# Kernel tuning notes

Measured on AMD Instinct MI355X. Metric: run time of the kernel, lower is better.

Reference implementation:

```python
import jax, jax.numpy as jnp
import numpy as np


def _lstm(x, Wx, Wh, b):
    """Fused-gate LSTM over time axis 1. x: [B,T,I]; Wx: [I,4H]; Wh: [H,4H]; b: [4H].
    Gate order (i, f, g, o) as in flax.linen.LSTMCell. Zero initial carry."""
    B, T, _ = x.shape
    H = Wh.shape[0]
    # Precompute all input-to-gate contributions in one big GEMM.
    xg = jnp.einsum('bti,ih->bth', x, Wx) + b  # [B,T,4H]

    def step(carry, xt):
        c, h = carry
        z = xt + h @ Wh  # [B,4H]
        i, f, g, o = jnp.split(z, 4, axis=-1)
        c = jax.nn.sigmoid(f) * c + jax.nn.sigmoid(i) * jnp.tanh(g)
        h = jax.nn.sigmoid(o) * jnp.tanh(c)
        return (c, h), h

    init = (jnp.zeros((B, H), x.dtype), jnp.zeros((B, H), x.dtype))
    _, hs = jax.lax.scan(step, init, jnp.swapaxes(xg, 0, 1))  # hs: [T,B,H]
    return jnp.swapaxes(hs, 0, 1)  # [B,T,H]


def _forward(X, conv_w, conv_b,
             Wx1, Wh1, b1, Wx2, Wh2, b2, Wx3, Wh3, b3, Wx4, Wh4, b4,
             Wa, ba, Va, bva, Wd1, bd1, Wd2, bd2):
    # 1-D conv, SAME padding (flax default), NWC layout.
    x = jax.lax.conv_general_dilated(X, conv_w, (1,), 'SAME',
                                     dimension_numbers=('NWC', 'WIO', 'NWC')) + conv_b
    # NOTE: source uses jnp.flip(..., axis=-1) -> flips FEATURE axis (faithful to source).
    x1 = _lstm(x, Wx1, Wh1, b1)
    x2 = _lstm(jnp.flip(x, axis=-1), Wx2, Wh2, b2)
    x = jnp.concatenate([x1, x2], axis=-1)  # [B,T,2F]
    x1 = _lstm(x, Wx3, Wh3, b3)
    x2 = _lstm(jnp.flip(x, axis=-1), Wx4, Wh4, b4)
    enc = jnp.concatenate([x1, x2], axis=-1)  # [B,T,4F]
    # Additive attention: softmax over time axis.
    score = jnp.tanh(enc @ Wa + ba) @ Va + bva  # [B,T,1]
    w = jax.nn.softmax(score, axis=1)
    ctx = jnp.sum(w * enc, axis=1)  # [B,4F]
    # MLP head (dropout deterministic -> identity).
    h = jnp.tanh(ctx @ Wd1 + bd1)
    return h @ Wd2 + bd2  # [B,1]


def setup_inputs() -> dict:
    key = jax.random.key(0)
    B, T, Cin, F = 32, 4096, 8, 64
    ks = iter(jax.random.split(key, 32))

    def w(shape):
        fan_in = shape[0] if len(shape) <= 2 else shape[0] * shape[1]
        return jax.random.normal(next(ks), shape, jnp.float32) / np.sqrt(fan_in)

    d = {}
    d['X'] = jax.random.normal(next(ks), (B, T, Cin), jnp.float32)
    d['conv_w'] = w((4, Cin, 16))
    d['conv_b'] = jnp.zeros((16,), jnp.float32)
    lstm_dims = {'1': (16, F), '2': (16, F), '3': (2 * F, 2 * F), '4': (2 * F, 2 * F)}
    for n, (i_dim, h_dim) in lstm_dims.items():
        d['Wx' + n] = w((i_dim, 4 * h_dim))
        d['Wh' + n] = w((h_dim, 4 * h_dim))
        d['b' + n] = jnp.zeros((4 * h_dim,), jnp.float32)
    d['Wa'] = w((4 * F, F)); d['ba'] = jnp.zeros((F,), jnp.float32)
    d['Va'] = w((F, 1));     d['bva'] = jnp.zeros((1,), jnp.float32)
    d['Wd1'] = w((4 * F, F)); d['bd1'] = jnp.zeros((F,), jnp.float32)
    d['Wd2'] = w((F, 1));     d['bd2'] = jnp.zeros((1,), jnp.float32)
    d['deterministic'] = 1
    return d


def reference(X, conv_w, conv_b,
              Wx1, Wh1, b1, Wx2, Wh2, b2, Wx3, Wh3, b3, Wx4, Wh4, b4,
              Wa, ba, Va, bva, Wd1, bd1, Wd2, bd2, deterministic):
    # deterministic=1 -> dropout is the identity; already reflected in _forward.
    return _forward(X, conv_w, conv_b,
                    Wx1, Wh1, b1, Wx2, Wh2, b2, Wx3, Wh3, b3, Wx4, Wh4, b4,
                    Wa, ba, Va, bva, Wd1, bd1, Wd2, bd2)
```

## Files before the change

### kernel.cpp

```cpp
#include <hip/hip_runtime.h>


#define TFULL 4096
#define NB 32

__device__ __forceinline__ float fexp2(float x){ return __builtin_amdgcn_exp2f(x); }
__device__ __forceinline__ float frcp(float x){ return __builtin_amdgcn_rcpf(x); }
__device__ __forceinline__ float sigf(float x){ return frcp(1.f + fexp2(-1.44269504f*x)); }
__device__ __forceinline__ float tanh_(float x){
    float e = fexp2(fminf(2.88539008f*x, 126.f));
    return (e - 1.f) * frcp(e + 1.f);
}
#define PIN4(v) asm volatile("" : "+v"(v.x), "+v"(v.y), "+v"(v.z), "+v"(v.w))

__global__ __launch_bounds__(256) void k_init(float* __restrict__ st1,
        float* __restrict__ st2, float* __restrict__ am, float* __restrict__ al,
        float* __restrict__ acc){
    int i = blockIdx.x * 256 + threadIdx.x;
    if (i < 8192)  st1[i] = 0.f;
    if (i < 16384) st2[i] = 0.f;
    if (i < 8192)  acc[i] = 0.f;
    if (i < 32){ am[i] = -3.4e38f; al[i] = 0.f; }
}

__global__ __launch_bounds__(256) void k_pack(
        const float* __restrict__ Wx1, const float* __restrict__ Wh1, const float* __restrict__ b1,
        const float* __restrict__ Wx2, const float* __restrict__ Wh2, const float* __restrict__ b2,
        const float* __restrict__ Wx3, const float* __restrict__ Wh3, const float* __restrict__ b3,
        const float* __restrict__ Wx4, const float* __restrict__ Wh4, const float* __restrict__ b4,
        float* __restrict__ W34, float* __restrict__ b34, float* __restrict__ W2p,
        float* __restrict__ W1p, float* __restrict__ b12){
    int i0 = blockIdx.x * 256 + threadIdx.x;
    int stride = gridDim.x * 256;
    for (int e = i0; e < 131072; e += stride){
        int k = e >> 10, n = e & 1023;
        W34[e] = (n < 512) ? Wx3[k*512 + n] : Wx4[(127 - k)*512 + (n - 512)];
    }
    for (int e = i0; e < 1024; e += stride) b34[e] = (e < 512) ? b3[e] : b4[e - 512];
    for (int e = i0; e < 131072; e += stride){
        int l = e >> 16, f = e & 65535;
        int p = f >> 14, g = f & 16383, tid = g >> 5, kk = g & 31;
        int q = tid & 127, s = tid >> 7;
        W2p[e] = (l ? Wh4 : Wh3)[(32*s + kk)*512 + 4*q + p];
    }
    for (int e = i0; e < 65536; e += stride){
        int l = e >> 15, r = e & 32767, tid = r >> 6, wq = r & 63;
        int q = tid & 63, s = tid >> 6;
        float v = 0.f;
        if (wq < 32){
            int c = wq >> 3, k = wq & 7;
            v = (l ? Wh2 : Wh1)[(s*8 + k)*256 + (4*q + c)];
        } else if (s < 2){
            int c = (wq - 32) >> 3, rr = (wq - 32) & 7;
            int rg = s*8 + rr, col = 4*q + c;
            v = l ? Wx2[(15 - rg)*256 + col] : Wx1[rg*256 + col];
        }
        W1p[e] = v;
    }
    for (int e = i0; e < 512; e += stride) b12[e] = (e < 256) ? b1[e] : b2[e - 256];
}

__global__ __launch_bounds__(256) void k_conv(const float* __restrict__ X,
        const float* __restrict__ W, const float* __restrict__ Bv,
        float* __restrict__ out, int t0, int lc){
    __shared__ float Ws[512];
    __shared__ float bs[16];
    int tid = threadIdx.x;
    Ws[tid] = W[tid]; Ws[tid + 256] = W[tid + 256];
    if (tid < 16) bs[tid] = Bv[tid];
    __syncthreads();
    int m = blockIdx.x * 256 + tid;
    int b = m >> lc, trel = m & ((1 << lc) - 1);
    int t = t0 + trel;
    float o[16];
    #pragma unroll
    for (int co = 0; co < 16; ++co) o[co] = bs[co];
    #pragma unroll
    for (int w = 0; w < 4; ++w){
        int tt = t + w - 1;
        if (tt >= 0 && tt < TFULL){
            const float* xr = X + ((size_t)(b << 12) + tt) * 8;
            #pragma unroll
            for (int ci = 0; ci < 8; ++ci){
                float v = xr[ci];
                #pragma unroll
                for (int co = 0; co < 16; ++co) o[co] += v * Ws[(w*8 + ci)*16 + co];
            }
        }
    }
    float* op = out + (size_t)m * 16;
    #pragma unroll
    for (int q = 0; q < 4; ++q)
        *(float4*)(op + q*4) = make_float4(o[q*4], o[q*4+1], o[q*4+2], o[q*4+3]);
}

__global__ void __launch_bounds__(512, 1)
k_scan1(const float* __restrict__ x, const float* __restrict__ W1p,
        const float* __restrict__ b12,
        float* __restrict__ cc, float* __restrict__ st1, int C){
    int l = blockIdx.x >> 5;
    int b = blockIdx.x & 31;
    int tid = threadIdx.x;
    int q = tid & 63;
    int s = tid >> 6;
    float4 w[16];
    {
        const float4* wp = (const float4*)(W1p + ((size_t)l*512 + tid)*64);
        #pragma unroll
        for (int i = 0; i < 16; ++i) w[i] = wp[i];
        #pragma unroll
        for (int i = 0; i < 16; ++i) PIN4(w[i]);
    }
    float bi0 = 0.f, bi1 = 0.f, bi2 = 0.f, bi3 = 0.f;
    if (tid < 64){
        bi0 = b12[l*256 + tid];       bi1 = b12[l*256 + 64 + tid];
        bi2 = b12[l*256 + 128 + tid]; bi3 = b12[l*256 + 192 + tid];
    }

    __shared__ float xs[128 * 16];
    __shared__ float zp[8 * 256];
    __shared__ float ccbuf[128 * 64];
    __shared__ float hbufs[64];
    float c = 0.f;
    int sidx = (l*32 + b)*64 + q;
    if (tid < 64){ c = st1[sidx]; hbufs[tid] = st1[4096 + sidx]; }
    __syncthreads();

    const float* xb = x + ((size_t)b * C) * 16;
    float* ccb = cc + ((size_t)b * C) * 128 + (l << 6);
    int BS = C < 128 ? C : 128;
    int bsm = BS - 1;
    int fr = tid >> 2, fi = tid & 3;

    #pragma clang loop unroll(disable)
    for (int t = 0; t < C; ++t){
        int st = t & bsm;
        if (st == 0){
            __syncthreads();
            if (t && fr < BS){
                const float4* cb4 = (const float4*)ccbuf + fr*16 + fi*4;
                float4* cgp = (float4*)(ccb + (size_t)(t - BS + fr)*128) + fi*4;
                #pragma unroll
                for (int i = 0; i < 4; ++i) cgp[i] = cb4[i];
            }
            if (tid < BS*4)
                ((float4*)xs)[tid] = ((const float4*)(xb + (size_t)t*16))[tid];
            __syncthreads();
        }
        float a0 = 0.f, a1 = 0.f, a2 = 0.f, a3 = 0.f;
        const float4* hb4 = (const float4*)hbufs + (s << 1);
        #pragma unroll
        for (int k4 = 0; k4 < 2; ++k4){
            float4 hv = hb4[k4];
            a0 = fmaf(hv.x, w[k4].x, a0);     a0 = fmaf(hv.y, w[k4].y, a0);
            a0 = fmaf(hv.z, w[k4].z, a0);     a0 = fmaf(hv.w, w[k4].w, a0);
            a1 = fmaf(hv.x, w[2+k4].x, a1);   a1 = fmaf(hv.y, w[2+k4].y, a1);
            a1 = fmaf(hv.z, w[2+k4].z, a1);   a1 = fmaf(hv.w, w[2+k4].w, a1);
            a2 = fmaf(hv.x, w[4+k4].x, a2);   a2 = fmaf(hv.y, w[4+k4].y, a2);
            a2 = fmaf(hv.z, w[4+k4].z, a2);   a2 = fmaf(hv.w, w[4+k4].w, a2);
            a3 = fmaf(hv.x, w[6+k4].x, a3);   a3 = fmaf(hv.y, w[6+k4].y, a3);
            a3 = fmaf(hv.z, w[6+k4].z, a3);   a3 = fmaf(hv.w, w[6+k4].w, a3);
        }
        if (s < 2){
            const float4* xr = (const float4*)(xs + st * 16) + (s << 1);
            #pragma unroll
            for (int r4 = 0; r4 < 2; ++r4){
                float4 xv = xr[r4];
                a0 = fmaf(xv.x, w[8+r4].x, a0);    a0 = fmaf(xv.y, w[8+r4].y, a0);
                a0 = fmaf(xv.z, w[8+r4].z, a0);    a0 = fmaf(xv.w, w[8+r4].w, a0);
                a1 = fmaf(xv.x, w[10+r4].x, a1);   a1 = fmaf(xv.y, w[10+r4].y, a1);
                a1 = fmaf(xv.z, w[10+r4].z, a1);   a1 = fmaf(xv.w, w[10+r4].w, a1);
                a2 = fmaf(xv.x, w[12+r4].x, a2);   a2 = fmaf(xv.y, w[12+r4].y, a2);
                a2 = fmaf(xv.z, w[12+r4].z, a2);   a2 = fmaf(xv.w, w[12+r4].w, a2);
                a3 = fmaf(xv.x, w[14+r4].x, a3);   a3 = fmaf(xv.y, w[14+r4].y, a3);
                a3 = fmaf(xv.z, w[14+r4].z, a3);   a3 = fmaf(xv.w, w[14+r4].w, a3);
            }
        }
        *(float4*)(zp + (s << 8) + (q << 2)) = make_float4(a0, a1, a2, a3);
        __syncthreads();
        if (tid < 64){
            float zi = bi0, zf = bi1, zg = bi2, zo = bi3;
            #pragma unroll
            for (int ss = 0; ss < 8; ++ss){
                const float* zr = zp + (ss << 8);
                zi += zr[tid]; zf += zr[64 + tid]; zg += zr[128 + tid]; zo += zr[192 + tid];
            }
            c = sigf(zf) * c + sigf(zi) * tanh_(zg);
            float h = sigf(zo) * tanh_(c);
            hbufs[tid] = h;
            ccbuf[st*64 + tid] = h;
        }
        __syncthreads();
    }
    if (fr < BS){
        const float4* cb4 = (const float4*)ccbuf + fr*16 + fi*4;
        float4* cgp = (float4*)(ccb + (size_t)(C - BS + fr)*128) + fi*4;
        #pragma unroll
        for (int i = 0; i < 4; ++i) cgp[i] = cb4[i];
    }
    if (tid < 64){ st1[sidx] = c; st1[4096 + sidx] = hbufs[tid]; }
}

template<bool TANH>
__global__ __launch_bounds__(128) void k_gemm(
        const float* __restrict__ A, int lda,
        const float* __restrict__ B, int ldb,
        const float* __restrict__ bias,
        float* __restrict__ Cm, int ldc, int K){
    __shared__ float As[64 * 129];
    __shared__ float Bs[64 * 68];
    int tid = threadIdx.x;
    int tx = tid & 7;
    int ty = tid >> 3;
    int r0 = blockIdx.x * 128;
    int n0 = blockIdx.y * 64;
    float acc[8][8];
    #pragma unroll
    for (int i = 0; i < 8; ++i)
        #pragma unroll
        for (int n = 0; n < 8; ++n) acc[i][n] = 0.f;

    for (int kb = 0; kb < K; kb += 64){
        __syncthreads();
        for (int idx = tid; idx < 2048; idx += 128){
            int r = idx >> 4, k4 = idx & 15;
            float4 v = *(const float4*)(A + (size_t)(r0 + r) * lda + kb + k4*4);
            As[(k4*4 + 0)*129 + r] = v.x;
            As[(k4*4 + 1)*129 + r] = v.y;
            As[(k4*4 + 2)*129 + r] = v.z;
            As[(k4*4 + 3)*129 + r] = v.w;
        }
        for (int idx = tid; idx < 1024; idx += 128){
            int n4 = idx & 15, k = idx >> 4;
            float4 v = *(const float4*)(B + (size_t)(kb + k) * ldb + n0 + n4*4);
            *(float4*)(Bs + k*68 + n4*4) = v;
        }
        __syncthreads();
        #pragma unroll 4
        for (int k = 0; k < 64; ++k){
            float a[8];
            #pragma unroll
            for (int i = 0; i < 8; ++i) a[i] = As[k*129 + ty*8 + i];
            float4 b0 = *(const float4*)(Bs + k*68 + tx*8);
            float4 b1 = *(const float4*)(Bs + k*68 + tx*8 + 4);
            float bq[8] = {b0.x, b0.y, b0.z, b0.w, b1.x, b1.y, b1.z, b1.w};
            #pragma unroll
            for (int i = 0; i < 8; ++i)
                #pragma unroll
                for (int n = 0; n < 8; ++n) acc[i][n] += a[i] * bq[n];
        }
    }
    #pragma unroll
    for (int i = 0; i < 8; ++i){
        size_t rr = (size_t)r0 + ty*8 + i;
        float* cp = Cm + rr * ldc + n0 + tx*8;
        float ov[8];
        #pragma unroll
        for (int n = 0; n < 8; ++n){
            float v = acc[i][n] + bias[n0 + tx*8 + n];
            ov[n] = TANH ? tanh_(v) : v;
        }
        *(float4*)cp       = make_float4(ov[0], ov[1], ov[2], ov[3]);
        *(float4*)(cp + 4) = make_float4(ov[4], ov[5], ov[6], ov[7]);
    }
}

__global__ void __launch_bounds__(512, 1)
k_scan2(const float* __restrict__ xg, const float* __restrict__ W2p,
        float* __restrict__ enc, float* __restrict__ st2, int C){
    int l = blockIdx.x >> 5;
    int b = blockIdx.x & 31;
    int tid = threadIdx.x;
    int q = tid & 127;
    int s = tid >> 7;

    __shared__ float smem[16384 + 4096 + 2048 + 128];
    float* xgbuf  = smem;
    float* encbuf = smem + 16384;
    float* zp     = smem + 20480;
    float* hbufs  = smem + 22528;

    float c = 0.f;
    int sidx = (l*32 + b)*128 + q;
    if (tid < 128){ c = st2[sidx]; hbufs[tid] = st2[8192 + sidx]; }

    float4 w[32];
    const float* Wg = W2p + (size_t)l * 65536;
    for (int p = 0; p < 4; ++p){
        __syncthreads();
        const float4* src4 = (const float4*)(Wg + p * 16384);
        float4* dst4 = (float4*)xgbuf;
        #pragma unroll
        for (int v = 0; v < 8; ++v) dst4[v*512 + tid] = src4[v*512 + tid];
        __syncthreads();
        const float4* ws4 = (const float4*)xgbuf + tid*8;
        #pragma unroll
        for (int j = 0; j < 8; ++j) w[p*8 + j] = ws4[j];
    }
    #pragma unroll
    for (int i = 0; i < 32; ++i) PIN4(w[i]);

    const float* xgg = xg + ((size_t)b * C) * 1024 + (l << 9);
    float* encb = enc + ((size_t)b * C) * 256 + (l << 7);
    int tq = tid & 15, tr = tid >> 4;

    #pragma clang loop unroll(disable)
    for (int t = 0; t < C; ++t){
        int st = t & 31;
        if (st == 0){
            __syncthreads();
            if (t){
                const float4* eb4 = (const float4*)encbuf + tr*32;
                float* eg = encb + (size_t)(t - 32 + tr) * 256;
                #pragma unroll
                for (int i = 0; i < 2; ++i)
                    *(float4*)(eg + (tq + i*16)*4) = eb4[tq + i*16];
            }
            {
                const float4* xs4 = (const float4*)(xgg + (size_t)(t + tr) * 1024);
                float4* xb4 = (float4*)xgbuf + tr*128;
                #pragma unroll
                for (int i = 0; i < 8; ++i)
                    xb4[tq + i*16] = xs4[tq + i*16];
            }
            __syncthreads();
        }
        float a0, a1, a2, a3;
        if (s == 0){
            float4 xv = *((const float4*)(xgbuf + st*512) + q);
            a0 = xv.x; a1 = xv.y; a2 = xv.z; a3 = xv.w;
        } else { a0 = a1 = a2 = a3 = 0.f; }
        const float4* hb4 = (const float4*)hbufs + (s << 3);
        #pragma unroll
        for (int k4 = 0; k4 < 8; ++k4){
            float4 hv = hb4[k4];
            a0 = fmaf(hv.x, w[k4].x, a0);      a0 = fmaf(hv.y, w[k4].y, a0);
            a0 = fmaf(hv.z, w[k4].z, a0);      a0 = fmaf(hv.w, w[k4].w, a0);
            a1 = fmaf(hv.x, w[8+k4].x, a1);    a1 = fmaf(hv.y, w[8+k4].y, a1);
            a1 = fmaf(hv.z, w[8+k4].z, a1);    a1 = fmaf(hv.w, w[8+k4].w, a1);
            a2 = fmaf(hv.x, w[16+k4].x, a2);   a2 = fmaf(hv.y, w[16+k4].y, a2);
            a2 = fmaf(hv.z, w[16+k4].z, a2);   a2 = fmaf(hv.w, w[16+k4].w, a2);
            a3 = fmaf(hv.x, w[24+k4].x, a3);   a3 = fmaf(hv.y, w[24+k4].y, a3);
            a3 = fmaf(hv.z, w[24+k4].z, a3);   a3 = fmaf(hv.w, w[24+k4].w, a3);
        }
        *(float4*)(zp + (s << 9) + (q << 2)) = make_float4(a0, a1, a2, a3);
        __syncthreads();
        if (tid < 128){
            float zi = zp[tid]       + zp[512 + tid]  + zp[1024 + tid] + zp[1536 + tid];
            float zf = zp[128 + tid] + zp[640 + tid]  + zp[1152 + tid] + zp[1664 + tid];
            float zg = zp[256 + tid] + zp[768 + tid]  + zp[1280 + tid] + zp[1792 + tid];
            float zo = zp[384 + tid] + zp[896 + tid]  + zp[1408 + tid] + zp[1920 + tid];
            c = sigf(zf) * c + sigf(zi) * tanh_(zg);
            float h = sigf(zo) * tanh_(c);
            hbufs[tid] = h;
            encbuf[st*128 + tid] = h;
        }
        __syncthreads();
    }
    {
        const float4* eb4 = (const float4*)encbuf + tr*32;
        float* eg = encb + (size_t)(C - 32 + tr) * 256;
        #pragma unroll
        for (int i = 0; i < 2; ++i)
            *(float4*)(eg + (tq + i*16)*4) = eb4[tq + i*16];
    }
    if (tid < 128){ st2[sidx] = c; st2[8192 + sidx] = hbufs[tid]; }
}

__global__ __launch_bounds__(256) void k_scorev(const float* __restrict__ u,
        const float* __restrict__ Va, const float* __restrict__ bva,
        float* __restrict__ sc){
    int m = blockIdx.x * 256 + threadIdx.x;
    const float4* up = (const float4*)(u + (size_t)m * 64);
    const float4* vp = (const float4*)Va;
    float acc = 0.f;
    #pragma unroll
    for (int i = 0; i < 16; ++i){
        float4 v = up[i], w = vp[i];
        acc += v.x*w.x + v.y*w.y + v.z*w.z + v.w*w.w;
    }
    sc[m] = acc + bva[0];
}

__global__ __launch_bounds__(1024) void k_attn(const float* __restrict__ sc,
        const float* __restrict__ enc, float* __restrict__ am,
        float* __restrict__ al, float* __restrict__ acc, int C){
    int b = blockIdx.x, tid = threadIdx.x;
    __shared__ float es[1024];
    __shared__ float red[16];
    __shared__ float sh[2];
    const float* sp = sc + (size_t)b * C;
    float mloc = -3.4e38f;
    for (int t = tid; t < C; t += 1024) mloc = fmaxf(mloc, sp[t]);
    #pragma unroll
    for (int off = 32; off; off >>= 1) mloc = fmaxf(mloc, __shfl_down(mloc, off));
    if ((tid & 63) == 0) red[tid >> 6] = mloc;
    __syncthreads();
    if (tid == 0){
        float mc = -3.4e38f;
        #pragma unroll
        for (int i = 0; i < 16; ++i) mc = fmaxf(mc, red[i]);
        float mo = am[b];
        float mn = fmaxf(mo, mc);
        sh[0] = mn;
        sh[1] = fexp2(1.44269504f * (mo - mn));
        am[b] = mn;
    }
    __syncthreads();
    float mn = sh[0], alpha = sh[1];
    float eloc = 0.f;
    for (int t = tid; t < C; t += 1024){
        float e = fexp2(1.44269504f * (sp[t] - mn));
        es[t] = e; eloc += e;
    }
    #pragma unroll
    for (int off = 32; off; off >>= 1) eloc += __shfl_down(eloc, off);
    if ((tid & 63) == 0) red[tid >> 6] = eloc;
    __syncthreads();
    if (tid == 0){
        float sm = 0.f;
        #pragma unroll
        for (int i = 0; i < 16; ++i) sm += red[i];
        al[b] = al[b] * alpha + sm;
    }
    int jf = tid & 255, sl = tid >> 8;
    int tlen = C >> 2;
    const float* ep = enc + ((size_t)b * C + (size_t)sl * tlen) * 256 + jf;
    const float* eb = es + sl * tlen;
    float a = 0.f;
    for (int t = 0; t < tlen; ++t) a = fmaf(eb[t], ep[(size_t)t * 256], a);
    __syncthreads();
    es[tid] = a;
    __syncthreads();
    if (tid < 256)
        acc[b*256 + tid] = acc[b*256 + tid] * alpha
                         + ((es[tid] + es[256 + tid]) + (es[512 + tid] + es[768 + tid]));
}

__global__ __launch_bounds__(256) void k_head(const float* __restrict__ acc,
        const float* __restrict__ al,
        const float* __restrict__ Wd1, const float* __restrict__ bd1,
        const float* __restrict__ Wd2, const float* __restrict__ bd2,
        float* __restrict__ out){
    __shared__ float ctxs[32 * 256];
    __shared__ float h1s[32 * 64];
    int tid = threadIdx.x;
    for (int idx = tid; idx < 8192; idx += 256){
        int b = idx >> 8;
        ctxs[idx] = acc[idx] / al[b];
    }
    __syncthreads();
    for (int idx = tid; idx < 2048; idx += 256){
        int b = idx >> 6, n = idx & 63;
        float a = bd1[n];
        for (int i = 0; i < 256; ++i) a += ctxs[b*256 + i] * Wd1[i*64 + n];
        h1s[idx] = tanh_(a);
    }
    __syncthreads();
    if (tid < 32){
        float a = bd2[0];
        #pragma unroll
        for (int n = 0; n < 64; ++n) a += h1s[tid*64 + n] * Wd2[n];
        out[tid] = a;
    }
}

extern "C" void kernel_launch(void* const* d_in, const int* in_sizes, int n_in,
                              void* d_out, int out_size, void* d_ws, size_t ws_size,
                              hipStream_t stream){
    const float* X     = (const float*)d_in[0];
    const float* convw = (const float*)d_in[1];
    const float* convb = (const float*)d_in[2];
    const float* Wx1 = (const float*)d_in[3];
    const float* Wh1 = (const float*)d_in[4];
    const float* b1  = (const float*)d_in[5];
    const float* Wx2 = (const float*)d_in[6];
    const float* Wh2 = (const float*)d_in[7];
    const float* b2  = (const float*)d_in[8];
    const float* Wx3 = (const float*)d_in[9];
    const float* Wh3 = (const float*)d_in[10];
    const float* b3  = (const float*)d_in[11];
    const float* Wx4 = (const float*)d_in[12];
    const float* Wh4 = (const float*)d_in[13];
    const float* b4  = (const float*)d_in[14];
    const float* Wa  = (const float*)d_in[15];
    const float* ba  = (const float*)d_in[16];
    const float* Va  = (const float*)d_in[17];
    const float* bva = (const float*)d_in[18];
    const float* Wd1 = (const float*)d_in[19];
    const float* bd1 = (const float*)d_in[20];
    const float* Wd2 = (const float*)d_in[21];
    const float* bd2 = (const float*)d_in[22];
    float* out = (float*)d_out;
    (void)in_sizes; (void)n_in; (void)out_size;

    const size_t fixedFl = 131072 + 1024 + 131072 + 65536 + 512
                         + 8192 + 16384 + 32 + 32 + 8192 + 32*1024;
    size_t capFl = ws_size / 4;
    int C = 1024;
    while (C > 32){
        size_t need = fixedFl + (size_t)NB * C * (16 + 128 + 1024 + 256 + 64);
        if (need <= capFl) break;
        C >>= 1;
    }
    int lc = 31 - __builtin_clz((unsigned)C);
    int nch = TFULL / C;

    float* ws   = (float*)d_ws;
    float* W34  = ws;
    float* b34  = W34 + 131072;
    float* W2p  = b34 + 1024;
    float* W1p  = W2p + 131072;
    float* b12  = W1p + 65536;
    float* st1  = b12 + 512;
    float* st2  = st1 + 8192;
    float* am   = st2 + 16384;
    float* al   = am + 32;
    float* acc  = al + 32;
    float* scb  = acc + 8192;
    float* xcv  = scb + 32*1024;
    float* ccb  = xcv + (size_t)NB*C*16;
    float* xgb  = ccb + (size_t)NB*C*128;
    float* enb  = xgb + (size_t)NB*C*1024;
    float* ub   = enb + (size_t)NB*C*256;

    k_init<<<64, 256, 0, stream>>>(st1, st2, am, al, acc);
    k_pack<<<512, 256, 0, stream>>>(Wx1, Wh1, b1, Wx2, Wh2, b2,
                                    Wx3, Wh3, b3, Wx4, Wh4, b4,
                                    W34, b34, W2p, W1p, b12);

    for (int ch = 0; ch < nch; ++ch){
        int t0 = ch * C;
        k_conv<<<NB*C/256, 256, 0, stream>>>(X, convw, convb, xcv, t0, lc);
        k_scan1<<<64, 512, 0, stream>>>(xcv, W1p, b12, ccb, st1, C);
        k_gemm<false><<<dim3(NB*C/128, 16), 128, 0, stream>>>(
            ccb, 128, W34, 1024, b34, xgb, 1024, 128);
        k_scan2<<<64, 512, 0, stream>>>(xgb, W2p, enb, st2, C);
        k_gemm<true><<<dim3(NB*C/128, 1), 128, 0, stream>>>(
            enb, 256, Wa, 64, ba, ub, 64, 256);
        k_scorev<<<NB*C/256, 256, 0, stream>>>(ub, Va, bva, scb);
        k_attn<<<32, 1024, 0, stream>>>(scb, enb, am, al, acc, C);
    }
    k_head<<<1, 256, 0, stream>>>(acc, al, Wd1, bd1, Wd2, bd2, out);
}
```

Measured before the change: 5.783 ms.

## Widen scan2 to 1024 threads and parallelize gate activations across all gate lanes

k_scan2 now runs 1024 threads per block, each holding 16 weight float4s in registers instead of 32. The weight packing changes to an 8-way K split with 16 rows per thread, and the weights load directly from global memory rather than being staged through shared memory. Both scans add a stage where 256 or 512 threads each reduce one gate pre-activation and apply sigmoid or tanh into shared memory, so only the cell update stays on the 64 or 128 state threads. This shortens the serial per-step critical path but adds a barrier per timestep and more partial sums to reduce.

```diff
diff --git a/kernel.cpp b/kernel.cpp
--- a/kernel.cpp
+++ b/kernel.cpp
@@ -38,10 +38,10 @@
     }
     for (int e = i0; e < 1024; e += stride) b34[e] = (e < 512) ? b3[e] : b4[e - 512];
     for (int e = i0; e < 131072; e += stride){
-        int l = e >> 16, f = e & 65535;
-        int p = f >> 14, g = f & 16383, tid = g >> 5, kk = g & 31;
+        int l = e >> 16, r = e & 65535, tid = r >> 6, widx = r & 63;
         int q = tid & 127, s = tid >> 7;
-        W2p[e] = (l ? Wh4 : Wh3)[(32*s + kk)*512 + 4*q + p];
+        int m = widx >> 4, kk = widx & 15;
+        W2p[e] = (l ? Wh4 : Wh3)[(16*s + kk)*512 + 4*q + m];
     }
     for (int e = i0; e < 65536; e += stride){
         int l = e >> 15, r = e & 32767, tid = r >> 6, wq = r & 63;
@@ -94,7 +94,7 @@
         *(float4*)(op + q*4) = make_float4(o[q*4], o[q*4+1], o[q*4+2], o[q*4+3]);
 }
 
-__global__ void __launch_bounds__(512, 1)
+__global__ void __launch_bounds__(512, 2)
 k_scan1(const float* __restrict__ x, const float* __restrict__ W1p,
         const float* __restrict__ b12,
         float* __restrict__ cc, float* __restrict__ st1, int C){
@@ -111,14 +111,11 @@
         #pragma unroll
         for (int i = 0; i < 16; ++i) PIN4(w[i]);
     }
-    float bi0 = 0.f, bi1 = 0.f, bi2 = 0.f, bi3 = 0.f;
-    if (tid < 64){
-        bi0 = b12[l*256 + tid];       bi1 = b12[l*256 + 64 + tid];
-        bi2 = b12[l*256 + 128 + tid]; bi3 = b12[l*256 + 192 + tid];
-    }
+    float bval = (tid < 256) ? b12[l*256 + tid] : 0.f;
 
     __shared__ float xs[128 * 16];
     __shared__ float zp[8 * 256];
+    __shared__ float actb[256];
     __shared__ float ccbuf[128 * 64];
     __shared__ float hbufs[64];
     float c = 0.f;
@@ -178,15 +175,18 @@
         }
         *(float4*)(zp + (s << 8) + (q << 2)) = make_float4(a0, a1, a2, a3);
         __syncthreads();
+        if (tid < 256){
+            float z = bval;
+            #pragma unroll
+            for (int ss = 0; ss < 8; ++ss) z += zp[(ss << 8) + tid];
+            actb[tid] = (tid >> 6) == 2 ? tanh_(z) : sigf(z);
+        }
+        __syncthreads();
         if (tid < 64){
-            float zi = bi0, zf = bi1, zg = bi2, zo = bi3;
-            #pragma unroll
-            for (int ss = 0; ss < 8; ++ss){
-                const float* zr = zp + (ss << 8);
-                zi += zr[tid]; zf += zr[64 + tid]; zg += zr[128 + tid]; zo += zr[192 + tid];
-            }
-            c = sigf(zf) * c + sigf(zi) * tanh_(zg);
-            float h = sigf(zo) * tanh_(c);
+            float gi = actb[tid], gf = actb[64 + tid];
+            float gg = actb[128 + tid], go = actb[192 + tid];
+            c = gf * c + gi * gg;
+            float h = go * tanh_(c);
             hbufs[tid] = h;
             ccbuf[st*64 + tid] = h;
         }
@@ -265,7 +265,7 @@
     }
 }
 
-__global__ void __launch_bounds__(512, 1)
+__global__ void __launch_bounds__(1024, 4)
 k_scan2(const float* __restrict__ xg, const float* __restrict__ W2p,
         float* __restrict__ enc, float* __restrict__ st2, int C){
     int l = blockIdx.x >> 5;
@@ -273,36 +273,29 @@
     int tid = threadIdx.x;
     int q = tid & 127;
     int s = tid >> 7;
-
-    __shared__ float smem[16384 + 4096 + 2048 + 128];
-    float* xgbuf  = smem;
-    float* encbuf = smem + 16384;
-    float* zp     = smem + 20480;
-    float* hbufs  = smem + 22528;
+    float4 w[16];
+    {
+        const float4* wp = (const float4*)(W2p + ((size_t)l*1024 + tid)*64);
+        #pragma unroll
+        for (int i = 0; i < 16; ++i) w[i] = wp[i];
+        #pragma unroll
+        for (int i = 0; i < 16; ++i) PIN4(w[i]);
+    }
+
+    __shared__ float xgbuf[32 * 512];
+    __shared__ float encbuf[32 * 128];
+    __shared__ float zp[8 * 512];
+    __shared__ float actb[512];
+    __shared__ float hbufs[128];
 
     float c = 0.f;
     int sidx = (l*32 + b)*128 + q;
     if (tid < 128){ c = st2[sidx]; hbufs[tid] = st2[8192 + sidx]; }
-
-    float4 w[32];
-    const float* Wg = W2p + (size_t)l * 65536;
-    for (int p = 0; p < 4; ++p){
-        __syncthreads();
-        const float4* src4 = (const float4*)(Wg + p * 16384);
-        float4* dst4 = (float4*)xgbuf;
-        #pragma unroll
-        for (int v = 0; v < 8; ++v) dst4[v*512 + tid] = src4[v*512 + tid];
-        __syncthreads();
-        const float4* ws4 = (const float4*)xgbuf + tid*8;
-        #pragma unroll
-        for (int j = 0; j < 8; ++j) w[p*8 + j] = ws4[j];
-    }
-    #pragma unroll
-    for (int i = 0; i < 32; ++i) PIN4(w[i]);
+    __syncthreads();
 
     const float* xgg = xg + ((size_t)b * C) * 1024 + (l << 9);
     float* encb = enc + ((size_t)b * C) * 256 + (l << 7);
-    int tq = tid & 15, tr = tid >> 4;
+    int tq = tid & 31, tr = tid >> 5;
 
     #pragma clang loop unroll(disable)
     for (int t = 0; t < C; ++t){
@@ -310,59 +303,53 @@
         if (st == 0){
             __syncthreads();
             if (t){
-                const float4* eb4 = (const float4*)encbuf + tr*32;
-                float* eg = encb + (size_t)(t - 32 + tr) * 256;
-                #pragma unroll
-                for (int i = 0; i < 2; ++i)
-                    *(float4*)(eg + (tq + i*16)*4) = eb4[tq + i*16];
+                float4 ev = *((const float4*)encbuf + tr*32 + tq);
+                *((float4*)(encb + (size_t)(t - 32 + tr) * 256) + tq) = ev;
             }
             {
                 const float4* xs4 = (const float4*)(xgg + (size_t)(t + tr) * 1024);
                 float4* xb4 = (float4*)xgbuf + tr*128;
                 #pragma unroll
-                for (int i = 0; i < 8; ++i)
-                    xb4[tq + i*16] = xs4[tq + i*16];
+                for (int i = 0; i < 4; ++i) xb4[tq + i*32] = xs4[tq + i*32];
             }
             __syncthreads();
         }
-        float a0, a1, a2, a3;
-        if (s == 0){
-            float4 xv = *((const float4*)(xgbuf + st*512) + q);
-            a0 = xv.x; a1 = xv.y; a2 = xv.z; a3 = xv.w;
-        } else { a0 = a1 = a2 = a3 = 0.f; }
-        const float4* hb4 = (const float4*)hbufs + (s << 3);
-        #pragma unroll
-        for (int k4 = 0; k4 < 8; ++k4){
+        float a0 = 0.f, a1 = 0.f, a2 = 0.f, a3 = 0.f;
+        const float4* hb4 = (const float4*)hbufs + (s << 2);
+        #pragma unroll
+        for (int k4 = 0; k4 < 4; ++k4){
             float4 hv = hb4[k4];
             a0 = fmaf(hv.x, w[k4].x, a0);      a0 = fmaf(hv.y, w[k4].y, a0);
             a0 = fmaf(hv.z, w[k4].z, a0);      a0 = fmaf(hv.w, w[k4].w, a0);
-            a1 = fmaf(hv.x, w[8+k4].x, a1);    a1 = fmaf(hv.y, w[8+k4].y, a1);
-            a1 = fmaf(hv.z, w[8+k4].z, a1);    a1 = fmaf(hv.w, w[8+k4].w, a1);
-            a2 = fmaf(hv.x, w[16+k4].x, a2);   a2 = fmaf(hv.y, w[16+k4].y, a2);
-            a2 = fmaf(hv.z, w[16+k4].z, a2);   a2 = fmaf(hv.w, w[16+k4].w, a2);
-            a3 = fmaf(hv.x, w[24+k4].x, a3);   a3 = fmaf(hv.y, w[24+k4].y, a3);
-            a3 = fmaf(hv.z, w[24+k4].z, a3);   a3 = fmaf(hv.w, w[24+k4].w, a3);
+            a1 = fmaf(hv.x, w[4+k4].x, a1);    a1 = fmaf(hv.y, w[4+k4].y, a1);
+            a1 = fmaf(hv.z, w[4+k4].z, a1);    a1 = fmaf(hv.w, w[4+k4].w, a1);
+            a2 = fmaf(hv.x, w[8+k4].x, a2);    a2 = fmaf(hv.y, w[8+k4].y, a2);
+            a2 = fmaf(hv.z, w[8+k4].z, a2);    a2 = fmaf(hv.w, w[8+k4].w, a2);
+            a3 = fmaf(hv.x, w[12+k4].x, a3);   a3 = fmaf(hv.y, w[12+k4].y, a3);
+            a3 = fmaf(hv.z, w[12+k4].z, a3);   a3 = fmaf(hv.w, w[12+k4].w, a3);
         }
         *(float4*)(zp + (s << 9) + (q << 2)) = make_float4(a0, a1, a2, a3);
         __syncthreads();
+        if (tid < 512){
+            float z = xgbuf[st*512 + tid];
+            #pragma unroll
+            for (int ss = 0; ss < 8; ++ss) z += zp[(ss << 9) + tid];
+            actb[tid] = (tid >> 7) == 2 ? tanh_(z) : sigf(z);
+        }
+        __syncthreads();
         if (tid < 128){
-            float zi = zp[tid]       + zp[512 + tid]  + zp[1024 + tid] + zp[1536 + tid];
-            float zf = zp[128 + tid] + zp[640 + tid]  + zp[1152 + tid] + zp[1664 + tid];
-            float zg = zp[256 + tid] + zp[768 + tid]  + zp[1280 + tid] + zp[1792 + tid];
-            float zo = zp[384 + tid] + zp[896 + tid]  + zp[1408 + tid] + zp[1920 + tid];
-            c = sigf(zf) * c + sigf(zi) * tanh_(zg);
-            float h = sigf(zo) * tanh_(c);
+            float gi = actb[tid], gf = actb[128 + tid];
+            float gg = actb[256 + tid], go = actb[384 + tid];
+            c = gf * c + gi * gg;
+            float h = go * tanh_(c);
             hbufs[tid] = h;
             encbuf[st*128 + tid] = h;
         }
         __syncthreads();
     }
     {
-        const float4* eb4 = (const float4*)encbuf + tr*32;
-        float* eg = encb + (size_t)(C - 32 + tr) * 256;
-        #pragma unroll
-        for (int i = 0; i < 2; ++i)
-            *(float4*)(eg + (tq + i*16)*4) = eb4[tq + i*16];
+        float4 ev = *((const float4*)encbuf + tr*32 + tq);
+        *((float4*)(encb + (size_t)(C - 32 + tr) * 256) + tq) = ev;
     }
     if (tid < 128){ st2[sidx] = c; st2[8192 + sidx] = hbufs[tid]; }
 }
@@ -535,7 +522,7 @@
         k_scan1<<<64, 512, 0, stream>>>(xcv, W1p, b12, ccb, st1, C);
         k_gemm<false><<<dim3(NB*C/128, 16), 128, 0, stream>>>(
             ccb, 128, W34, 1024, b34, xgb, 1024, 128);
-        k_scan2<<<64, 512, 0, stream>>>(xgb, W2p, enb, st2, C);
+        k_scan2<<<64, 1024, 0, stream>>>(xgb, W2p, enb, st2, C);
         k_gemm<true><<<dim3(NB*C/128, 1), 128, 0, stream>>>(
             enb, 256, Wa, 64, ba, ub, 64, 256);
         k_scorev<<<NB*C/256, 256, 0, stream>>>(ub, Va, bva, scb);
```

Measured after the change: 5.844 ms. No clear change (+1.1%).
